# Kernel tuning notes

Measured on AMD Instinct MI355X. Metric: run time of the kernel, lower is better.

## Reference

```python
import jax, jax.numpy as jnp
import numpy as np

B, N, M, C = 256, 2048, 64, 512
OUT = 3 * M + 6  # fc_write output: [M,1,1,3,1,M,M]


def setup_inputs() -> dict:
    key = jax.random.key(0)
    k0, k1, k2, k3, k4 = jax.random.split(key, 5)
    xavier = 1.4 * np.sqrt(6.0 / (C + OUT))  # xavier_uniform gain=1.4 scale
    return {
        "h": jax.random.normal(k0, (B, C), jnp.float32),
        "w_prev": jax.nn.softmax(jax.random.normal(k1, (B, N), jnp.float32), axis=1),
        "memory": jax.random.normal(k2, (B, N, M), jnp.float32),
        "W": jax.random.uniform(k3, (OUT, C), jnp.float32, -xavier, xavier),
        "b": 0.01 * jax.random.normal(k4, (OUT,), jnp.float32),
    }


def reference(h, w_prev, memory, W, b):
    # controller projection + split
    o = h @ W.T + b  # [B, 3M+6]
    bounds = np.cumsum([M, 1, 1, 3, 1, M])
    k, beta, g, s, gamma, e, a = jnp.split(o, bounds, axis=1)
    beta = jax.nn.softplus(beta)            # [B,1]
    g = jax.nn.sigmoid(g)                   # [B,1]
    s = jax.nn.softmax(s, axis=1)           # [B,3] shift weights {-1,0,+1}
    gamma = 1.0 + jax.nn.softplus(gamma)    # [B,1]
    e = jax.nn.sigmoid(e)                   # [B,M]

    # content addressing: cosine similarity + softmax
    mem_e = memory + 1e-16
    k_e = k + 1e-16
    sim = jnp.einsum('bnm,bm->bn', mem_e, k_e)
    denom = jnp.maximum(
        jnp.linalg.norm(mem_e, axis=-1) * jnp.linalg.norm(k_e, axis=-1, keepdims=True),
        1e-8,
    )
    w_c = jax.nn.softmax(beta * sim / denom, axis=1)  # [B,N]

    # interpolation gate
    w_g = g * w_c + (1.0 - g) * w_prev

    # circular shift convolution (3 taps)
    w_t = (jnp.roll(w_g, 1, axis=1) * s[:, 0:1]
           + w_g * s[:, 1:2]
           + jnp.roll(w_g, -1, axis=1) * s[:, 2:3])

    # sharpening
    w_s = w_t ** gamma
    w = w_s / (jnp.sum(w_s, axis=1, keepdims=True) + 1e-16)  # [B,N]

    # erase/add memory write
    erase = jnp.einsum('bn,bm->bnm', w, e)
    add = jnp.einsum('bn,bm->bnm', w, a)
    mem_new = memory * (1.0 - erase) + add
    return w, mem_new
```

## Files before the change

kernel.cpp:

```cpp
#include <hip/hip_runtime.h>
#include <stdint.h>

#define BB   256
#define NN   2048
#define MM   64
#define CC   512
#define OUTD 198

#define PSTRIDE   256
#define K_OFF     0
#define E_OFF     64
#define A_OFF     128
#define BETA_OFF  192
#define G_OFF     193
#define GAMMA_OFF 194
#define S_OFF     195
#define KNORM_OFF 198
#define LOGITS_OFF (BB * PSTRIDE)

typedef float vf4 __attribute__((ext_vector_type(4)));

__device__ __forceinline__ float softplusf(float x) {
    return x > 20.f ? x : log1pf(expf(x));
}
__device__ __forceinline__ float sigmoidf(float x) {
    return 1.f / (1.f + expf(-x));
}

__global__ __launch_bounds__(256) void k_ctrl(
        const float* __restrict__ h, const float* __restrict__ Wm,
        const float* __restrict__ bias, float* __restrict__ ws) {
    __shared__ float hs[CC];
    __shared__ float os[OUTD];
    const int b = blockIdx.x, t = threadIdx.x;

    for (int c = t; c < CC; c += 256) hs[c] = h[b * CC + c];
    __syncthreads();

    if (t < OUTD) {
        const float* wr = Wm + (size_t)t * CC;
        float acc = 0.f;
        #pragma unroll 8
        for (int c = 0; c < CC; c += 4) {
            float4 p = *(const float4*)(wr + c);
            acc += p.x * hs[c+0] + p.y * hs[c+1] + p.z * hs[c+2] + p.w * hs[c+3];
        }
        os[t] = acc + bias[t];
    }
    __syncthreads();

    float* P = ws + (size_t)b * PSTRIDE;
    if (t < 64) {
        P[K_OFF + t] = os[t];
    } else if (t == 64) {
        P[BETA_OFF] = softplusf(os[64]);
    } else if (t == 65) {
        P[G_OFF] = sigmoidf(os[65]);
    } else if (t == 66) {
        float x0 = os[66], x1 = os[67], x2 = os[68];
        float mx = fmaxf(x0, fmaxf(x1, x2));
        float e0 = expf(x0 - mx), e1 = expf(x1 - mx), e2 = expf(x2 - mx);
        float inv = 1.f / (e0 + e1 + e2);
        P[S_OFF + 0] = e0 * inv; P[S_OFF + 1] = e1 * inv; P[S_OFF + 2] = e2 * inv;
    } else if (t == 69) {
        P[GAMMA_OFF] = 1.f + softplusf(os[69]);
    } else if (t >= 70 && t < 134) {
        P[E_OFF + (t - 70)] = sigmoidf(os[t]);
    } else if (t >= 134 && t < 198) {
        P[A_OFF + (t - 134)] = os[t];
    } else if (t == 198) {
        float ss = 0.f;
        for (int i = 0; i < MM; ++i) { float kv = os[i] + 1e-16f; ss += kv * kv; }
        P[KNORM_OFF] = sqrtf(ss);
    }
}

__global__ __launch_bounds__(256) void k_logits(
        const float* __restrict__ mem, float* __restrict__ ws) {
    const int b = blockIdx.x >> 3;
    const int chunk = blockIdx.x & 7;
    const int t = threadIdx.x;
    const int l = t & 15;
    const int grp = t >> 4;

    const float* P = ws + (size_t)b * PSTRIDE;
    float kv[4];
    #pragma unroll
    for (int i = 0; i < 4; ++i) kv[i] = P[K_OFF + 4 * l + i] + 1e-16f;
    const float beta  = P[BETA_OFF];
    const float knorm = P[KNORM_OFF];
    float* lg = ws + LOGITS_OFF + (size_t)b * NN;

    const int row0 = chunk * 256;
    #pragma unroll
    for (int it = 0; it < 16; ++it) {
        const int row = row0 + it * 16 + grp;
        float4 p = *(const float4*)(mem + ((size_t)b * NN + row) * MM + 4 * l);
        float m0 = p.x + 1e-16f, m1 = p.y + 1e-16f, m2 = p.z + 1e-16f, m3 = p.w + 1e-16f;
        float dot = m0 * kv[0] + m1 * kv[1] + m2 * kv[2] + m3 * kv[3];
        float ss  = m0 * m0 + m1 * m1 + m2 * m2 + m3 * m3;
        #pragma unroll
        for (int off = 1; off < 16; off <<= 1) {
            dot += __shfl_xor(dot, off, 64);
            ss  += __shfl_xor(ss,  off, 64);
        }
        if (l == 0) {
            float denom = fmaxf(sqrtf(ss) * knorm, 1e-8f);
            lg[row] = beta * dot / denom;
        }
    }
}

__device__ __forceinline__ float bred_max(float v, float* red) {
    #pragma unroll
    for (int off = 32; off; off >>= 1) v = fmaxf(v, __shfl_down(v, off, 64));
    if ((threadIdx.x & 63) == 0) red[threadIdx.x >> 6] = v;
    __syncthreads();
    float r = fmaxf(fmaxf(red[0], red[1]), fmaxf(red[2], red[3]));
    __syncthreads();
    return r;
}
__device__ __forceinline__ float bred_sum(float v, float* red) {
    #pragma unroll
    for (int off = 32; off; off >>= 1) v += __shfl_down(v, off, 64);
    if ((threadIdx.x & 63) == 0) red[threadIdx.x >> 6] = v;
    __syncthreads();
    float r = red[0] + red[1] + red[2] + red[3];
    __syncthreads();
    return r;
}

__global__ __launch_bounds__(256) void k_addr(
        const float* __restrict__ w_prev, float* __restrict__ ws,
        float* __restrict__ w_out) {
    __shared__ float buf[NN];
    __shared__ float buf2[NN];
    __shared__ float red[4];
    const int b = blockIdx.x, t = threadIdx.x;
    const float* P  = ws + (size_t)b * PSTRIDE;
    const float* lg = ws + LOGITS_OFF + (size_t)b * NN;

    const float g  = P[G_OFF];
    const float s0 = P[S_OFF + 0], s1 = P[S_OFF + 1], s2 = P[S_OFF + 2];
    const float gamma = P[GAMMA_OFF];

    float v[8];
    float lmax = -1e30f;
    #pragma unroll
    for (int i = 0; i < 8; ++i) { v[i] = lg[t + i * 256]; lmax = fmaxf(lmax, v[i]); }
    lmax = bred_max(lmax, red);

    float lsum = 0.f;
    #pragma unroll
    for (int i = 0; i < 8; ++i) { v[i] = expf(v[i] - lmax); lsum += v[i]; }
    lsum = bred_sum(lsum, red);
    const float inv = 1.f / lsum;

    #pragma unroll
    for (int i = 0; i < 8; ++i) {
        const int n = t + i * 256;
        float wc = v[i] * inv;
        buf[n] = g * wc + (1.f - g) * w_prev[(size_t)b * NN + n];
    }
    __syncthreads();

    float psum = 0.f;
    #pragma unroll
    for (int i = 0; i < 8; ++i) {
        const int n = t + i * 256;
        float wt = buf[(n + NN - 1) & (NN - 1)] * s0 + buf[n] * s1
                 + buf[(n + 1) & (NN - 1)] * s2;
        float wsv = (wt > 0.f) ? exp2f(gamma * log2f(wt)) : 0.f;
        buf2[n] = wsv;
        psum += wsv;
    }
    psum = bred_sum(psum, red);
    const float invp = 1.f / (psum + 1e-16f);

    #pragma unroll
    for (int i = 0; i < 8; ++i) {
        const int n = t + i * 256;
        w_out[(size_t)b * NN + n] = buf2[n] * invp;
    }
}

__global__ __launch_bounds__(256) void k_write(
        const float* __restrict__ mem, const float* __restrict__ ws,
        const float* __restrict__ w_in, float* __restrict__ out_mem) {
    const size_t tid0 = (size_t)blockIdx.x * 256 + threadIdx.x;
    #pragma unroll
    for (int rep = 0; rep < 8; ++rep) {
        const size_t u = tid0 + (size_t)rep * (4096u * 256u);
        const size_t base = u * 4;
        const int b = (int)(base >> 17);
        const int n = (int)(base >> 6) & (NN - 1);
        const int m = (int)base & (MM - 1);

        const float w = w_in[((size_t)b << 11) + n];
        const float* P = ws + (size_t)b * PSTRIDE;
        float4 p = *(const float4*)(mem + base);

        vf4 o;
        o.x = p.x * (1.f - w * P[E_OFF + m + 0]) + w * P[A_OFF + m + 0];
        o.y = p.y * (1.f - w * P[E_OFF + m + 1]) + w * P[A_OFF + m + 1];
        o.z = p.z * (1.f - w * P[E_OFF + m + 2]) + w * P[A_OFF + m + 2];
        o.w = p.w * (1.f - w * P[E_OFF + m + 3]) + w * P[A_OFF + m + 3];
        __builtin_nontemporal_store(o, (vf4*)(out_mem + base));
    }
}

extern "C" void kernel_launch(void* const* d_in, const int* in_sizes, int n_in,
                              void* d_out, int out_size, void* d_ws, size_t ws_size,
                              hipStream_t stream) {
    const float* h      = (const float*)d_in[0];
    const float* w_prev = (const float*)d_in[1];
    const float* memory = (const float*)d_in[2];
    const float* W      = (const float*)d_in[3];
    const float* bias   = (const float*)d_in[4];
    float* out = (float*)d_out;
    float* ws = (float*)d_ws;

    float* w_out   = out;
    float* mem_out = out + (size_t)BB * NN;

    k_ctrl  <<<BB,     256, 0, stream>>>(h, W, bias, ws);
    k_logits<<<BB * 8, 256, 0, stream>>>(memory, ws);
    k_addr  <<<BB,     256, 0, stream>>>(w_prev, ws, w_out);
    k_write <<<4096,   256, 0, stream>>>(memory, ws, w_out, mem_out);
}
```

Measured before the change: 286.6 us.

## Fuse controller, addressing, and memory write into one per-batch kernel

Replaces the four kernels with a single 1024-thread block per batch row. That block computes the controller projection, the cosine logits, softmax, shift and sharpening, and the erase/add write, keeping intermediates in shared memory. The aim is to cut launch overhead and the global workspace round-trips. Because each block reads its 512KB memory slice twice, the second read may hit in L2/MALL. The risk is that only 256 blocks run and each has long serial phases, which can leave CUs underused and make it hard to overlap the logits and write phases across blocks.

```diff
diff --git a/kernel.cpp b/kernel.cpp
--- a/kernel.cpp
+++ b/kernel.cpp
@@ -7,17 +7,6 @@
 #define CC   512
 #define OUTD 198
 
-#define PSTRIDE   256
-#define K_OFF     0
-#define E_OFF     64
-#define A_OFF     128
-#define BETA_OFF  192
-#define G_OFF     193
-#define GAMMA_OFF 194
-#define S_OFF     195
-#define KNORM_OFF 198
-#define LOGITS_OFF (BB * PSTRIDE)
-
 typedef float vf4 __attribute__((ext_vector_type(4)));
 
 __device__ __forceinline__ float softplusf(float x) {
@@ -27,185 +16,171 @@
     return 1.f / (1.f + expf(-x));
 }
 
-__global__ __launch_bounds__(256) void k_ctrl(
+__global__ __launch_bounds__(1024, 4) void k_fused(
         const float* __restrict__ h, const float* __restrict__ Wm,
-        const float* __restrict__ bias, float* __restrict__ ws) {
+        const float* __restrict__ bias, const float* __restrict__ w_prev,
+        const float* __restrict__ mem, float* __restrict__ w_out,
+        float* __restrict__ mem_out) {
     __shared__ float hs[CC];
     __shared__ float os[OUTD];
-    const int b = blockIdx.x, t = threadIdx.x;
-
-    for (int c = t; c < CC; c += 256) hs[c] = h[b * CC + c];
-    __syncthreads();
-
-    if (t < OUTD) {
-        const float* wr = Wm + (size_t)t * CC;
+    __shared__ __align__(16) float kk[MM];
+    __shared__ __align__(16) float ee[MM];
+    __shared__ __align__(16) float aa[MM];
+    __shared__ float sc[8];
+    __shared__ float lg[NN];
+    __shared__ float wg[NN];
+    __shared__ float red[16];
+
+    const int b = blockIdx.x;
+    const int t = threadIdx.x;
+    const int lane = t & 63;
+    const int wid = t >> 6;
+
+    if (t < CC) hs[t] = h[(size_t)b * CC + t];
+    __syncthreads();
+
+    if (t < 4 * OUTD) {
+        const int row = t >> 2, l4 = t & 3;
+        const float* wr = Wm + (size_t)row * CC + 4 * l4;
         float acc = 0.f;
+        #pragma unroll
+        for (int c = 0; c < CC; c += 16) {
+            const float4 p = *(const float4*)(wr + c);
+            const int hb = c + 4 * l4;
+            acc += p.x * hs[hb] + p.y * hs[hb + 1] + p.z * hs[hb + 2] + p.w * hs[hb + 3];
+        }
+        acc += __shfl_xor(acc, 1, 64);
+        acc += __shfl_xor(acc, 2, 64);
+        if (l4 == 0) os[row] = acc + bias[row];
+    }
+    __syncthreads();
+
+    if (t < 64) {
+        const float kv = os[t] + 1e-16f;
+        kk[t] = kv;
+        float ss = kv * kv;
+        #pragma unroll
+        for (int off = 32; off; off >>= 1) ss += __shfl_xor(ss, off, 64);
+        if (t == 0) sc[3] = sqrtf(ss);
+    } else if (t < 128) {
+        const int m = t - 64;
+        ee[m] = sigmoidf(os[70 + m]);
+        aa[m] = os[134 + m];
+    } else if (t == 128) {
+        sc[0] = softplusf(os[64]);
+    } else if (t == 129) {
+        sc[1] = sigmoidf(os[65]);
+    } else if (t == 130) {
+        sc[2] = 1.f + softplusf(os[69]);
+    } else if (t == 131) {
+        const float x0 = os[66], x1 = os[67], x2 = os[68];
+        const float mx = fmaxf(x0, fmaxf(x1, x2));
+        const float e0 = expf(x0 - mx), e1 = expf(x1 - mx), e2 = expf(x2 - mx);
+        const float inv = 1.f / (e0 + e1 + e2);
+        sc[4] = e0 * inv; sc[5] = e1 * inv; sc[6] = e2 * inv;
+    }
+    __syncthreads();
+
+    {
+        const int l = t & 15, grp = t >> 4;
+        const float kv0 = kk[4 * l + 0], kv1 = kk[4 * l + 1];
+        const float kv2 = kk[4 * l + 2], kv3 = kk[4 * l + 3];
+        const float beta = sc[0], knorm = sc[3];
+        const float* mb = mem + (size_t)b * NN * MM;
+        #pragma unroll 4
+        for (int it = 0; it < 32; ++it) {
+            const int row = it * 64 + grp;
+            const float4 p = *(const float4*)(mb + (size_t)row * MM + 4 * l);
+            const float m0 = p.x + 1e-16f, m1 = p.y + 1e-16f;
+            const float m2 = p.z + 1e-16f, m3 = p.w + 1e-16f;
+            float dot = m0 * kv0 + m1 * kv1 + m2 * kv2 + m3 * kv3;
+            float ss  = m0 * m0 + m1 * m1 + m2 * m2 + m3 * m3;
+            #pragma unroll
+            for (int off = 1; off < 16; off <<= 1) {
+                dot += __shfl_xor(dot, off, 64);
+                ss  += __shfl_xor(ss,  off, 64);
+            }
+            if (l == 0)
+                lg[row] = beta * dot / fmaxf(sqrtf(ss) * knorm, 1e-8f);
+        }
+    }
+    __syncthreads();
+
+    const float g = sc[1], gamma = sc[2];
+    const float s0 = sc[4], s1 = sc[5], s2 = sc[6];
+
+    float v0 = lg[t], v1 = lg[t + 1024];
+    float lmax = fmaxf(v0, v1);
+    #pragma unroll
+    for (int off = 32; off; off >>= 1) lmax = fmaxf(lmax, __shfl_xor(lmax, off, 64));
+    if (lane == 0) red[wid] = lmax;
+    __syncthreads();
+    float mx = red[0];
+    #pragma unroll
+    for (int i = 1; i < 16; ++i) mx = fmaxf(mx, red[i]);
+    __syncthreads();
+
+    v0 = expf(v0 - mx); v1 = expf(v1 - mx);
+    float lsum = v0 + v1;
+    #pragma unroll
+    for (int off = 32; off; off >>= 1) lsum += __shfl_xor(lsum, off, 64);
+    if (lane == 0) red[wid] = lsum;
+    __syncthreads();
+    float tot = 0.f;
+    #pragma unroll
+    for (int i = 0; i < 16; ++i) tot += red[i];
+    __syncthreads();
+    const float inv = 1.f / tot;
+
+    wg[t]        = g * (v0 * inv) + (1.f - g) * w_prev[(size_t)b * NN + t];
+    wg[t + 1024] = g * (v1 * inv) + (1.f - g) * w_prev[(size_t)b * NN + t + 1024];
+    __syncthreads();
+
+    float ws0, ws1;
+    {
+        const int n0 = t;
+        const float wt0 = wg[(n0 + NN - 1) & (NN - 1)] * s0 + wg[n0] * s1
+                        + wg[(n0 + 1) & (NN - 1)] * s2;
+        ws0 = (wt0 > 0.f) ? exp2f(gamma * log2f(wt0)) : 0.f;
+        const int n1 = t + 1024;
+        const float wt1 = wg[(n1 - 1) & (NN - 1)] * s0 + wg[n1] * s1
+                        + wg[(n1 + 1) & (NN - 1)] * s2;
+        ws1 = (wt1 > 0.f) ? exp2f(gamma * log2f(wt1)) : 0.f;
+    }
+    float psum = ws0 + ws1;
+    #pragma unroll
+    for (int off = 32; off; off >>= 1) psum += __shfl_xor(psum, off, 64);
+    if (lane == 0) red[wid] = psum;
+    __syncthreads();
+    float ptot = 0.f;
+    #pragma unroll
+    for (int i = 0; i < 16; ++i) ptot += red[i];
+    const float invp = 1.f / (ptot + 1e-16f);
+
+    const float wf0 = ws0 * invp, wf1 = ws1 * invp;
+    lg[t] = wf0;
+    lg[t + 1024] = wf1;
+    w_out[(size_t)b * NN + t] = wf0;
+    w_out[(size_t)b * NN + t + 1024] = wf1;
+    __syncthreads();
+
+    {
+        const int m0 = (4 * t) & 63;
+        const vf4 ev = *(const vf4*)(ee + m0);
+        const vf4 av = *(const vf4*)(aa + m0);
+        const float* mb = mem + (size_t)b * NN * MM + 4 * t;
+        float* ob = mem_out + (size_t)b * NN * MM + 4 * t;
         #pragma unroll 8
-        for (int c = 0; c < CC; c += 4) {
-            float4 p = *(const float4*)(wr + c);
-            acc += p.x * hs[c+0] + p.y * hs[c+1] + p.z * hs[c+2] + p.w * hs[c+3];
+        for (int it = 0; it < 32; ++it) {
+            const float w = lg[it * 64 + (t >> 4)];
+            const float4 p = *(const float4*)(mb + it * 4096);
+            vf4 o;
+            o.x = p.x * (1.f - w * ev.x) + w * av.x;
+            o.y = p.y * (1.f - w * ev.y) + w * av.y;
+            o.z = p.z * (1.f - w * ev.z) + w * av.z;
+            o.w = p.w * (1.f - w * ev.w) + w * av.w;
+            __builtin_nontemporal_store(o, (vf4*)(ob + it * 4096));
         }
-        os[t] = acc + bias[t];
-    }
-    __syncthreads();
-
-    float* P = ws + (size_t)b * PSTRIDE;
-    if (t < 64) {
-        P[K_OFF + t] = os[t];
-    } else if (t == 64) {
-        P[BETA_OFF] = softplusf(os[64]);
-    } else if (t == 65) {
-        P[G_OFF] = sigmoidf(os[65]);
-    } else if (t == 66) {
-        float x0 = os[66], x1 = os[67], x2 = os[68];
-        float mx = fmaxf(x0, fmaxf(x1, x2));
-        float e0 = expf(x0 - mx), e1 = expf(x1 - mx), e2 = expf(x2 - mx);
-        float inv = 1.f / (e0 + e1 + e2);
-        P[S_OFF + 0] = e0 * inv; P[S_OFF + 1] = e1 * inv; P[S_OFF + 2] = e2 * inv;
-    } else if (t == 69) {
-        P[GAMMA_OFF] = 1.f + softplusf(os[69]);
-    } else if (t >= 70 && t < 134) {
-        P[E_OFF + (t - 70)] = sigmoidf(os[t]);
-    } else if (t >= 134 && t < 198) {
-        P[A_OFF + (t - 134)] = os[t];
-    } else if (t == 198) {
-        float ss = 0.f;
-        for (int i = 0; i < MM; ++i) { float kv = os[i] + 1e-16f; ss += kv * kv; }
-        P[KNORM_OFF] = sqrtf(ss);
-    }
-}
-
-__global__ __launch_bounds__(256) void k_logits(
-        const float* __restrict__ mem, float* __restrict__ ws) {
-    const int b = blockIdx.x >> 3;
-    const int chunk = blockIdx.x & 7;
-    const int t = threadIdx.x;
-    const int l = t & 15;
-    const int grp = t >> 4;
-
-    const float* P = ws + (size_t)b * PSTRIDE;
-    float kv[4];
-    #pragma unroll
-    for (int i = 0; i < 4; ++i) kv[i] = P[K_OFF + 4 * l + i] + 1e-16f;
-    const float beta  = P[BETA_OFF];
-    const float knorm = P[KNORM_OFF];
-    float* lg = ws + LOGITS_OFF + (size_t)b * NN;
-
-    const int row0 = chunk * 256;
-    #pragma unroll
-    for (int it = 0; it < 16; ++it) {
-        const int row = row0 + it * 16 + grp;
-        float4 p = *(const float4*)(mem + ((size_t)b * NN + row) * MM + 4 * l);
-        float m0 = p.x + 1e-16f, m1 = p.y + 1e-16f, m2 = p.z + 1e-16f, m3 = p.w + 1e-16f;
-        float dot = m0 * kv[0] + m1 * kv[1] + m2 * kv[2] + m3 * kv[3];
-        float ss  = m0 * m0 + m1 * m1 + m2 * m2 + m3 * m3;
-        #pragma unroll
-        for (int off = 1; off < 16; off <<= 1) {
-            dot += __shfl_xor(dot, off, 64);
-            ss  += __shfl_xor(ss,  off, 64);
-        }
-        if (l == 0) {
-            float denom = fmaxf(sqrtf(ss) * knorm, 1e-8f);
-            lg[row] = beta * dot / denom;
-        }
-    }
-}
-
-__device__ __forceinline__ float bred_max(float v, float* red) {
-    #pragma unroll
-    for (int off = 32; off; off >>= 1) v = fmaxf(v, __shfl_down(v, off, 64));
-    if ((threadIdx.x & 63) == 0) red[threadIdx.x >> 6] = v;
-    __syncthreads();
-    float r = fmaxf(fmaxf(red[0], red[1]), fmaxf(red[2], red[3]));
-    __syncthreads();
-    return r;
-}
-__device__ __forceinline__ float bred_sum(float v, float* red) {
-    #pragma unroll
-    for (int off = 32; off; off >>= 1) v += __shfl_down(v, off, 64);
-    if ((threadIdx.x & 63) == 0) red[threadIdx.x >> 6] = v;
-    __syncthreads();
-    float r = red[0] + red[1] + red[2] + red[3];
-    __syncthreads();
-    return r;
-}
-
-__global__ __launch_bounds__(256) void k_addr(
-        const float* __restrict__ w_prev, float* __restrict__ ws,
-        float* __restrict__ w_out) {
-    __shared__ float buf[NN];
-    __shared__ float buf2[NN];
-    __shared__ float red[4];
-    const int b = blockIdx.x, t = threadIdx.x;
-    const float* P  = ws + (size_t)b * PSTRIDE;
-    const float* lg = ws + LOGITS_OFF + (size_t)b * NN;
-
-    const float g  = P[G_OFF];
-    const float s0 = P[S_OFF + 0], s1 = P[S_OFF + 1], s2 = P[S_OFF + 2];
-    const float gamma = P[GAMMA_OFF];
-
-    float v[8];
-    float lmax = -1e30f;
-    #pragma unroll
-    for (int i = 0; i < 8; ++i) { v[i] = lg[t + i * 256]; lmax = fmaxf(lmax, v[i]); }
-    lmax = bred_max(lmax, red);
-
-    float lsum = 0.f;
-    #pragma unroll
-    for (int i = 0; i < 8; ++i) { v[i] = expf(v[i] - lmax); lsum += v[i]; }
-    lsum = bred_sum(lsum, red);
-    const float inv = 1.f / lsum;
-
-    #pragma unroll
-    for (int i = 0; i < 8; ++i) {
-        const int n = t + i * 256;
-        float wc = v[i] * inv;
-        buf[n] = g * wc + (1.f - g) * w_prev[(size_t)b * NN + n];
-    }
-    __syncthreads();
-
-    float psum = 0.f;
-    #pragma unroll
-    for (int i = 0; i < 8; ++i) {
-        const int n = t + i * 256;
-        float wt = buf[(n + NN - 1) & (NN - 1)] * s0 + buf[n] * s1
-                 + buf[(n + 1) & (NN - 1)] * s2;
-        float wsv = (wt > 0.f) ? exp2f(gamma * log2f(wt)) : 0.f;
-        buf2[n] = wsv;
-        psum += wsv;
-    }
-    psum = bred_sum(psum, red);
-    const float invp = 1.f / (psum + 1e-16f);
-
-    #pragma unroll
-    for (int i = 0; i < 8; ++i) {
-        const int n = t + i * 256;
-        w_out[(size_t)b * NN + n] = buf2[n] * invp;
-    }
-}
-
-__global__ __launch_bounds__(256) void k_write(
-        const float* __restrict__ mem, const float* __restrict__ ws,
-        const float* __restrict__ w_in, float* __restrict__ out_mem) {
-    const size_t tid0 = (size_t)blockIdx.x * 256 + threadIdx.x;
-    #pragma unroll
-    for (int rep = 0; rep < 8; ++rep) {
-        const size_t u = tid0 + (size_t)rep * (4096u * 256u);
-        const size_t base = u * 4;
-        const int b = (int)(base >> 17);
-        const int n = (int)(base >> 6) & (NN - 1);
-        const int m = (int)base & (MM - 1);
-
-        const float w = w_in[((size_t)b << 11) + n];
-        const float* P = ws + (size_t)b * PSTRIDE;
-        float4 p = *(const float4*)(mem + base);
-
-        vf4 o;
-        o.x = p.x * (1.f - w * P[E_OFF + m + 0]) + w * P[A_OFF + m + 0];
-        o.y = p.y * (1.f - w * P[E_OFF + m + 1]) + w * P[A_OFF + m + 1];
-        o.z = p.z * (1.f - w * P[E_OFF + m + 2]) + w * P[A_OFF + m + 2];
-        o.w = p.w * (1.f - w * P[E_OFF + m + 3]) + w * P[A_OFF + m + 3];
-        __builtin_nontemporal_store(o, (vf4*)(out_mem + base));
     }
 }
 
@@ -218,13 +193,9 @@
     const float* W      = (const float*)d_in[3];
     const float* bias   = (const float*)d_in[4];
     float* out = (float*)d_out;
-    float* ws = (float*)d_ws;
 
     float* w_out   = out;
     float* mem_out = out + (size_t)BB * NN;
 
-    k_ctrl  <<<BB,     256, 0, stream>>>(h, W, bias, ws);
-    k_logits<<<BB * 8, 256, 0, stream>>>(memory, ws);
-    k_addr  <<<BB,     256, 0, stream>>>(w_prev, ws, w_out);
-    k_write <<<4096,   256, 0, stream>>>(memory, ws, w_out, mem_out);
-}
+    k_fused<<<BB, 1024, 0, stream>>>(h, W, bias, w_prev, memory, w_out, mem_out);
+}
```

New measurement: 272.1 us. 1.05x faster.

## Fuse addressing and memory-write kernels with redundant per-quarter softmax recompute

Applied to the files above, without the earlier changes.

Merges the addressing (softmax, gate, shift, sharpen) kernel with the erase/add write kernel. Each batch row gets four 512-thread blocks; every block recomputes the full addressing weights redundantly into shared memory and then writes one quarter of that row's memory. This removes a kernel launch and the round trip of w through global memory, and gives the write phase 1024 blocks instead of a separate grid. The cost is four times the addressing work and the 2048-entry logits reads per row. It also adds occupancy hints to the logits kernel.

```diff
diff --git a/kernel.cpp b/kernel.cpp
--- a/kernel.cpp
+++ b/kernel.cpp
@@ -75,7 +75,7 @@
     }
 }
 
-__global__ __launch_bounds__(256) void k_logits(
+__global__ __launch_bounds__(256, 8) void k_logits(
         const float* __restrict__ mem, float* __restrict__ ws) {
     const int b = blockIdx.x >> 3;
     const int chunk = blockIdx.x & 7;
@@ -111,32 +111,18 @@
     }
 }
 
-__device__ __forceinline__ float bred_max(float v, float* red) {
-    #pragma unroll
-    for (int off = 32; off; off >>= 1) v = fmaxf(v, __shfl_down(v, off, 64));
-    if ((threadIdx.x & 63) == 0) red[threadIdx.x >> 6] = v;
-    __syncthreads();
-    float r = fmaxf(fmaxf(red[0], red[1]), fmaxf(red[2], red[3]));
-    __syncthreads();
-    return r;
-}
-__device__ __forceinline__ float bred_sum(float v, float* red) {
-    #pragma unroll
-    for (int off = 32; off; off >>= 1) v += __shfl_down(v, off, 64);
-    if ((threadIdx.x & 63) == 0) red[threadIdx.x >> 6] = v;
-    __syncthreads();
-    float r = red[0] + red[1] + red[2] + red[3];
-    __syncthreads();
-    return r;
-}
-
-__global__ __launch_bounds__(256) void k_addr(
-        const float* __restrict__ w_prev, float* __restrict__ ws,
-        float* __restrict__ w_out) {
+__global__ __launch_bounds__(512, 8) void k_addrwrite(
+        const float* __restrict__ w_prev, const float* __restrict__ ws,
+        const float* __restrict__ mem, float* __restrict__ w_out,
+        float* __restrict__ mem_out) {
     __shared__ float buf[NN];
-    __shared__ float buf2[NN];
-    __shared__ float red[4];
-    const int b = blockIdx.x, t = threadIdx.x;
+    __shared__ float wfin[NN];
+    __shared__ float red[8];
+    const int b = blockIdx.x >> 2;
+    const int q = blockIdx.x & 3;
+    const int t = threadIdx.x;
+    const int lane = t & 63, wid = t >> 6;
+
     const float* P  = ws + (size_t)b * PSTRIDE;
     const float* lg = ws + LOGITS_OFF + (size_t)b * NN;
 
@@ -144,68 +130,80 @@
     const float s0 = P[S_OFF + 0], s1 = P[S_OFF + 1], s2 = P[S_OFF + 2];
     const float gamma = P[GAMMA_OFF];
 
-    float v[8];
+    float v[4];
     float lmax = -1e30f;
     #pragma unroll
-    for (int i = 0; i < 8; ++i) { v[i] = lg[t + i * 256]; lmax = fmaxf(lmax, v[i]); }
-    lmax = bred_max(lmax, red);
+    for (int i = 0; i < 4; ++i) { v[i] = lg[t + i * 512]; lmax = fmaxf(lmax, v[i]); }
+    #pragma unroll
+    for (int off = 32; off; off >>= 1) lmax = fmaxf(lmax, __shfl_xor(lmax, off, 64));
+    if (lane == 0) red[wid] = lmax;
+    __syncthreads();
+    float mx = red[0];
+    #pragma unroll
+    for (int i = 1; i < 8; ++i) mx = fmaxf(mx, red[i]);
+    __syncthreads();
 
     float lsum = 0.f;
     #pragma unroll
-    for (int i = 0; i < 8; ++i) { v[i] = expf(v[i] - lmax); lsum += v[i]; }
-    lsum = bred_sum(lsum, red);
-    const float inv = 1.f / lsum;
-
-    #pragma unroll
-    for (int i = 0; i < 8; ++i) {
-        const int n = t + i * 256;
-        float wc = v[i] * inv;
-        buf[n] = g * wc + (1.f - g) * w_prev[(size_t)b * NN + n];
+    for (int i = 0; i < 4; ++i) { v[i] = expf(v[i] - mx); lsum += v[i]; }
+    #pragma unroll
+    for (int off = 32; off; off >>= 1) lsum += __shfl_xor(lsum, off, 64);
+    if (lane == 0) red[wid] = lsum;
+    __syncthreads();
+    float tot = 0.f;
+    #pragma unroll
+    for (int i = 0; i < 8; ++i) tot += red[i];
+    __syncthreads();
+    const float inv = 1.f / tot;
+
+    #pragma unroll
+    for (int i = 0; i < 4; ++i) {
+        const int n = t + i * 512;
+        buf[n] = g * (v[i] * inv) + (1.f - g) * w_prev[(size_t)b * NN + n];
     }
     __syncthreads();
 
     float psum = 0.f;
     #pragma unroll
-    for (int i = 0; i < 8; ++i) {
-        const int n = t + i * 256;
-        float wt = buf[(n + NN - 1) & (NN - 1)] * s0 + buf[n] * s1
-                 + buf[(n + 1) & (NN - 1)] * s2;
-        float wsv = (wt > 0.f) ? exp2f(gamma * log2f(wt)) : 0.f;
-        buf2[n] = wsv;
-        psum += wsv;
-    }
-    psum = bred_sum(psum, red);
-    const float invp = 1.f / (psum + 1e-16f);
-
-    #pragma unroll
-    for (int i = 0; i < 8; ++i) {
-        const int n = t + i * 256;
-        w_out[(size_t)b * NN + n] = buf2[n] * invp;
-    }
-}
-
-__global__ __launch_bounds__(256) void k_write(
-        const float* __restrict__ mem, const float* __restrict__ ws,
-        const float* __restrict__ w_in, float* __restrict__ out_mem) {
-    const size_t tid0 = (size_t)blockIdx.x * 256 + threadIdx.x;
-    #pragma unroll
-    for (int rep = 0; rep < 8; ++rep) {
-        const size_t u = tid0 + (size_t)rep * (4096u * 256u);
-        const size_t base = u * 4;
-        const int b = (int)(base >> 17);
-        const int n = (int)(base >> 6) & (NN - 1);
-        const int m = (int)base & (MM - 1);
-
-        const float w = w_in[((size_t)b << 11) + n];
-        const float* P = ws + (size_t)b * PSTRIDE;
-        float4 p = *(const float4*)(mem + base);
-
-        vf4 o;
-        o.x = p.x * (1.f - w * P[E_OFF + m + 0]) + w * P[A_OFF + m + 0];
-        o.y = p.y * (1.f - w * P[E_OFF + m + 1]) + w * P[A_OFF + m + 1];
-        o.z = p.z * (1.f - w * P[E_OFF + m + 2]) + w * P[A_OFF + m + 2];
-        o.w = p.w * (1.f - w * P[E_OFF + m + 3]) + w * P[A_OFF + m + 3];
-        __builtin_nontemporal_store(o, (vf4*)(out_mem + base));
+    for (int i = 0; i < 4; ++i) {
+        const int n = t + i * 512;
+        const float wt = buf[(n + NN - 1) & (NN - 1)] * s0 + buf[n] * s1
+                       + buf[(n + 1) & (NN - 1)] * s2;
+        v[i] = (wt > 0.f) ? exp2f(gamma * log2f(wt)) : 0.f;
+        psum += v[i];
+    }
+    #pragma unroll
+    for (int off = 32; off; off >>= 1) psum += __shfl_xor(psum, off, 64);
+    if (lane == 0) red[wid] = psum;
+    __syncthreads();
+    float ptot = 0.f;
+    #pragma unroll
+    for (int i = 0; i < 8; ++i) ptot += red[i];
+    const float invp = 1.f / (ptot + 1e-16f);
+
+    #pragma unroll
+    for (int i = 0; i < 4; ++i) wfin[t + i * 512] = v[i] * invp;
+    w_out[(size_t)b * NN + q * 512 + t] = v[q] * invp;
+    __syncthreads();
+
+    {
+        const int m0 = 4 * (t & 15);
+        const vf4 ev = *(const vf4*)(P + E_OFF + m0);
+        const vf4 av = *(const vf4*)(P + A_OFF + m0);
+        const size_t base = ((size_t)b * NN + (size_t)q * 512) * MM + 4 * t;
+        const float* mb = mem + base;
+        float* ob = mem_out + base;
+        #pragma unroll 4
+        for (int it = 0; it < 16; ++it) {
+            const float w = wfin[q * 512 + it * 32 + (t >> 4)];
+            const float4 p = *(const float4*)(mb + (size_t)it * 2048);
+            vf4 o;
+            o.x = p.x * (1.f - w * ev.x) + w * av.x;
+            o.y = p.y * (1.f - w * ev.y) + w * av.y;
+            o.z = p.z * (1.f - w * ev.z) + w * av.z;
+            o.w = p.w * (1.f - w * ev.w) + w * av.w;
+            __builtin_nontemporal_store(o, (vf4*)(ob + (size_t)it * 2048));
+        }
     }
 }
 
@@ -218,13 +216,12 @@
     const float* W      = (const float*)d_in[3];
     const float* bias   = (const float*)d_in[4];
     float* out = (float*)d_out;
-    float* ws = (float*)d_ws;
+    float* ws  = (float*)d_ws;
 
     float* w_out   = out;
     float* mem_out = out + (size_t)BB * NN;
 
-    k_ctrl  <<<BB,     256, 0, stream>>>(h, W, bias, ws);
-    k_logits<<<BB * 8, 256, 0, stream>>>(memory, ws);
-    k_addr  <<<BB,     256, 0, stream>>>(w_prev, ws, w_out);
-    k_write <<<4096,   256, 0, stream>>>(memory, ws, w_out, mem_out);
-}
+    k_ctrl     <<<BB,     256, 0, stream>>>(h, W, bias, ws);
+    k_logits   <<<BB * 8, 256, 0, stream>>>(memory, ws);
+    k_addrwrite<<<BB * 4, 512, 0, stream>>>(w_prev, ws, memory, w_out, mem_out);
+}
```

Result: no change. 283.1 us (-1.2%).
